# Optimization experiments

Hardware: AMD Instinct MI355X
Metric: run time of the kernel (lower is better)

The kernel has to match this reference:

```python
import jax, jax.numpy as jnp
import numpy as np

D_MODEL = 256
D_STATE = 2
BATCH = 8
SEQ = 8192


def setup_inputs() -> dict:
    key = jax.random.key(0)
    ks = jax.random.split(key, 8)
    s = 1.0 / np.sqrt(D_STATE)
    x = jax.random.normal(ks[0], (BATCH, SEQ, D_MODEL), dtype=jnp.float32)
    # stable range so exp(cumsum) stays finite at T=8192 (see notes)
    log_a_mag = -jax.random.uniform(ks[1], (D_MODEL, D_STATE), jnp.float32, 1e-5, 1e-3)
    a_phase = jax.random.uniform(ks[2], (D_MODEL, D_STATE), jnp.float32, 0.0, 2.0 * np.pi)
    B_re = jax.random.normal(ks[3], (D_MODEL, D_STATE), jnp.float32) * s
    B_im = jax.random.normal(ks[4], (D_MODEL, D_STATE), jnp.float32) * s
    C_re = jax.random.normal(ks[5], (D_MODEL, D_STATE), jnp.float32) * s
    C_im = jax.random.normal(ks[6], (D_MODEL, D_STATE), jnp.float32) * s
    D_diag = jnp.ones((D_MODEL,), jnp.float32)
    return dict(x=x, log_a_mag=log_a_mag, a_phase=a_phase, B_re=B_re, B_im=B_im,
                C_re=C_re, C_im=C_im, D_diag=D_diag)


def reference(x, log_a_mag, a_phase, B_re, B_im, C_re, C_im, D_diag):
    # x: (B, T, D); params: (D, S)
    Bsz, T, D = x.shape
    S = log_a_mag.shape[1]
    # cumulative complex log-decay along time, shape (D, S, T)
    cum_r = jnp.cumsum(jnp.broadcast_to(log_a_mag[:, :, None], (D, S, T)), axis=-1)
    cum_i = jnp.cumsum(jnp.broadcast_to(a_phase[:, :, None], (D, S, T)), axis=-1)
    x_t = jnp.swapaxes(x, 1, 2)                      # (B, D, T)
    Bu_r = B_re[None, :, :, None] * x_t[:, :, None, :]   # (B, D, S, T)
    Bu_i = B_im[None, :, :, None] * x_t[:, :, None, :]
    # exp(-cum_log_a): descale inputs
    en = jnp.exp(-cum_r)
    enr = en * jnp.cos(-cum_i)
    eni = en * jnp.sin(-cum_i)
    sr = enr * Bu_r - eni * Bu_i
    si = enr * Bu_i + eni * Bu_r
    csr = jnp.cumsum(sr, axis=-1)
    csi = jnp.cumsum(si, axis=-1)
    # exp(+cum_log_a): rescale prefix sums -> hidden states h (B, D, S, T)
    ec = jnp.exp(cum_r)
    ecr = ec * jnp.cos(cum_i)
    eci = ec * jnp.sin(cum_i)
    h_r = ecr * csr - eci * csi
    h_i = ecr * csi + eci * csr
    # output: Re(C . h) summed over state + skip D*x
    y = jnp.einsum('bdst,ds->bdt', h_r, C_re) - jnp.einsum('bdst,ds->bdt', h_i, C_im)
    y = jnp.swapaxes(y, 1, 2) + D_diag * x           # (B, T, D)
    return y
```

## Files before the change

kernel.cpp:

```cpp
#include <hip/hip_runtime.h>
#include <math.h>

#define BATCH  8
#define SEQ    8192
#define DMODEL 256
#define DSTATE 2
#define CHUNKS 256
#define CLEN   32
#define CPAD   1040
#define NSEG   16
#define SEGLEN 16


__global__ __launch_bounds__(256, 8)
void ssm_chunk_state(const float* __restrict__ x,
                     const float* __restrict__ lam,
                     const float* __restrict__ aph,
                     const float* __restrict__ Bre,
                     const float* __restrict__ Bim,
                     float* __restrict__ E) {
    const int d   = threadIdx.x;
    const int bid = blockIdx.x;
    const int b   = bid >> 8;
    const int c   = bid & (CHUNKS - 1);

    const float2 lm2 = *reinterpret_cast<const float2*>(lam + d * 2);
    const float2 ph2 = *reinterpret_cast<const float2*>(aph + d * 2);
    const float2 br2 = *reinterpret_cast<const float2*>(Bre + d * 2);
    const float2 bi2 = *reinterpret_cast<const float2*>(Bim + d * 2);
    const float m0 = expf(lm2.x), m1 = expf(lm2.y);
    const float ar0 = m0 * cosf(ph2.x), ai0 = m0 * sinf(ph2.x);
    const float ar1 = m1 * cosf(ph2.y), ai1 = m1 * sinf(ph2.y);
    const float br0 = br2.x, br1 = br2.y, bi0 = bi2.x, bi1 = bi2.y;

    float hr0 = 0.f, hi0 = 0.f, hr1 = 0.f, hi1 = 0.f;
    const float* xp = x + ((size_t)b * SEQ + (size_t)c * CLEN) * DMODEL + d;
#pragma unroll 8
    for (int t = 0; t < CLEN; ++t) {
        const float xt = xp[(size_t)t * DMODEL];
        const float bx0 = br0 * xt, by0 = bi0 * xt;
        const float bx1 = br1 * xt, by1 = bi1 * xt;
        const float n0r = fmaf(ar0, hr0, fmaf(-ai0, hi0, bx0));
        const float n0i = fmaf(ar0, hi0, fmaf( ai0, hr0, by0));
        const float n1r = fmaf(ar1, hr1, fmaf(-ai1, hi1, bx1));
        const float n1i = fmaf(ar1, hi1, fmaf( ai1, hr1, by1));
        hr0 = n0r; hi0 = n0i; hr1 = n1r; hi1 = n1i;
    }

    float4 ev;
    ev.x = hr0; ev.y = hi0; ev.z = hr1; ev.w = hi1;
    *reinterpret_cast<float4*>(E + ((size_t)b * CHUNKS + c) * CPAD + d * 4) = ev;
}

__global__ __launch_bounds__(256, 4)
void ssm_seg_aggregate(const float* __restrict__ E,
                       const float* __restrict__ lam,
                       const float* __restrict__ aph,
                       float* __restrict__ G) {
    const int bid  = blockIdx.x;
    const int b    = bid >> 5;
    const int seg  = (bid >> 1) & (NSEG - 1);
    const int r    = ((bid & 1) << 8) + threadIdx.x;
    const int d    = r >> 1;
    const int s    = r & 1;

    const double lm = (double)lam[d * 2 + s];
    const double ph = (double)aph[d * 2 + s];
    const double mL = exp(lm * (double)CLEN);
    const double pL = ph * (double)CLEN;
    const float Ar = (float)(mL * cos(pL));
    const float Ai = (float)(mL * sin(pL));

    const size_t ebase =
        ((size_t)b * CHUNKS + (size_t)seg * SEGLEN) * CPAD + (size_t)r * 2;

    float2 e[SEGLEN];
#pragma unroll
    for (int i = 0; i < SEGLEN; ++i)
        e[i] = *reinterpret_cast<const float2*>(E + ebase + (size_t)i * CPAD);

    float vr = e[0].x, vi = e[0].y;
#pragma unroll
    for (int i = 1; i < SEGLEN; ++i) {
        const float nr = fmaf(Ar, vr, fmaf(-Ai, vi, e[i].x));
        const float ni = fmaf(Ar, vi, fmaf( Ai, vr, e[i].y));
        vr = nr; vi = ni;
    }

    *reinterpret_cast<float2*>(G + (((size_t)b * NSEG + seg) * 512 + r) * 2) =
        make_float2(vr, vi);
}

__global__ __launch_bounds__(256, 4)
void ssm_seg_scan(const float* __restrict__ E,
                  const float* __restrict__ G,
                  const float* __restrict__ lam,
                  const float* __restrict__ aph,
                  float* __restrict__ Hin) {
    const int bid  = blockIdx.x;
    const int b    = bid >> 5;
    const int seg  = (bid >> 1) & (NSEG - 1);
    const int r    = ((bid & 1) << 8) + threadIdx.x;
    const int d    = r >> 1;
    const int s    = r & 1;

    const double lm = (double)lam[d * 2 + s];
    const double ph = (double)aph[d * 2 + s];
    const double mL = exp(lm * (double)CLEN);
    const double pL = ph * (double)CLEN;
    const float Ar = (float)(mL * cos(pL));
    const float Ai = (float)(mL * sin(pL));
    const double mS = exp(lm * (double)(CLEN * SEGLEN));
    const double pS = ph * (double)(CLEN * SEGLEN);
    const float Sr = (float)(mS * cos(pS));
    const float Si = (float)(mS * sin(pS));

    float2 g[NSEG];
#pragma unroll
    for (int k = 0; k < NSEG; ++k)
        g[k] = *reinterpret_cast<const float2*>(
            G + (((size_t)b * NSEG + k) * 512 + r) * 2);

    const size_t ebase =
        ((size_t)b * CHUNKS + (size_t)seg * SEGLEN) * CPAD + (size_t)r * 2;
    float2 e[SEGLEN];
#pragma unroll
    for (int i = 0; i < SEGLEN; ++i)
        e[i] = *reinterpret_cast<const float2*>(E + ebase + (size_t)i * CPAD);

    float pr = 0.f, pi = 0.f;
#pragma unroll
    for (int k = 0; k < NSEG; ++k) {
        if (k < seg) {
            const float nr = fmaf(Sr, pr, fmaf(-Si, pi, g[k].x));
            const float ni = fmaf(Sr, pi, fmaf( Si, pr, g[k].y));
            pr = nr; pi = ni;
        }
    }

#pragma unroll
    for (int i = 0; i < SEGLEN; ++i) {
        *reinterpret_cast<float2*>(Hin + ebase + (size_t)i * CPAD) =
            make_float2(pr, pi);
        const float nr = fmaf(Ar, pr, fmaf(-Ai, pi, e[i].x));
        const float ni = fmaf(Ar, pi, fmaf( Ai, pr, e[i].y));
        pr = nr; pi = ni;
    }
}

__global__ __launch_bounds__(256, 8)
void ssm_output(const float* __restrict__ x,
                const float* __restrict__ lam,
                const float* __restrict__ aph,
                const float* __restrict__ Bre,
                const float* __restrict__ Bim,
                const float* __restrict__ Cre,
                const float* __restrict__ Cim,
                const float* __restrict__ Dd,
                const float* __restrict__ Hin,
                float* __restrict__ y) {
    const int d   = threadIdx.x;
    const int bid = blockIdx.x;
    const int b   = bid >> 8;
    const int c   = bid & (CHUNKS - 1);

    const float4 hv = *reinterpret_cast<const float4*>(
        Hin + ((size_t)b * CHUNKS + c) * CPAD + d * 4);
    float hr0 = hv.x, hi0 = hv.y, hr1 = hv.z, hi1 = hv.w;

    const float2 lm2 = *reinterpret_cast<const float2*>(lam + d * 2);
    const float2 ph2 = *reinterpret_cast<const float2*>(aph + d * 2);
    const float2 br2 = *reinterpret_cast<const float2*>(Bre + d * 2);
    const float2 bi2 = *reinterpret_cast<const float2*>(Bim + d * 2);
    const float2 cr2 = *reinterpret_cast<const float2*>(Cre + d * 2);
    const float2 ci2 = *reinterpret_cast<const float2*>(Cim + d * 2);
    const float dd  = Dd[d];
    const float m0 = expf(lm2.x), m1 = expf(lm2.y);
    const float ar0 = m0 * cosf(ph2.x), ai0 = m0 * sinf(ph2.x);
    const float ar1 = m1 * cosf(ph2.y), ai1 = m1 * sinf(ph2.y);
    const float br0 = br2.x, br1 = br2.y, bi0 = bi2.x, bi1 = bi2.y;
    const float cr0 = cr2.x, cr1 = cr2.y, ci0 = ci2.x, ci1 = ci2.y;

    const size_t tbase = ((size_t)b * SEQ + (size_t)c * CLEN) * DMODEL + d;
    const float* xp = x + tbase;
    float* yp = y + tbase;
#pragma unroll 8
    for (int t = 0; t < CLEN; ++t) {
        const float xt = xp[(size_t)t * DMODEL];
        const float n0r = fmaf(ar0, hr0, fmaf(-ai0, hi0, br0 * xt));
        const float n0i = fmaf(ar0, hi0, fmaf( ai0, hr0, bi0 * xt));
        const float n1r = fmaf(ar1, hr1, fmaf(-ai1, hi1, br1 * xt));
        const float n1i = fmaf(ar1, hi1, fmaf( ai1, hr1, bi1 * xt));
        hr0 = n0r; hi0 = n0i; hr1 = n1r; hi1 = n1i;
        float acc = dd * xt;
        acc = fmaf(cr0, n0r, acc);
        acc = fmaf(-ci0, n0i, acc);
        acc = fmaf(cr1, n1r, acc);
        acc = fmaf(-ci1, n1i, acc);
        __builtin_nontemporal_store(acc, yp + (size_t)t * DMODEL);
    }
}

extern "C" void kernel_launch(void* const* d_in, const int* in_sizes, int n_in,
                              void* d_out, int out_size, void* d_ws, size_t ws_size,
                              hipStream_t stream) {
    const float* x   = (const float*)d_in[0];
    const float* lam = (const float*)d_in[1];
    const float* aph = (const float*)d_in[2];
    const float* Bre = (const float*)d_in[3];
    const float* Bim = (const float*)d_in[4];
    const float* Cre = (const float*)d_in[5];
    const float* Cim = (const float*)d_in[6];
    const float* Dd  = (const float*)d_in[7];
    float* yo = (float*)d_out;

    float* E   = (float*)d_ws;
    float* Hin = E + (size_t)BATCH * CHUNKS * CPAD;
    float* G   = Hin + (size_t)BATCH * CHUNKS * CPAD;

    ssm_chunk_state<<<BATCH * CHUNKS, 256, 0, stream>>>(x, lam, aph, Bre, Bim, E);
    ssm_seg_aggregate<<<BATCH * NSEG * 2, 256, 0, stream>>>(E, lam, aph, G);
    ssm_seg_scan<<<BATCH * NSEG * 2, 256, 0, stream>>>(E, G, lam, aph, Hin);
    ssm_output<<<BATCH * CHUNKS, 256, 0, stream>>>(x, lam, aph, Bre, Bim,
                                                   Cre, Cim, Dd, Hin, yo);
}
```

Baseline: 145.2 us.

## Fuse segment scan into output kernel, recomputing chunk prefix per block

Removes the separate seg_scan kernel and the Hin workspace. Each output block now rebuilds its own starting state by scanning the segment aggregates G and the earlier chunk states E in its segment. It derives the chunk and segment decay powers by repeated double-precision squaring of the per-step decay. This saves one launch and a full write and read of Hin, but adds up to about 30 serial dependent loads and FMAs per block before the main loop, plus some double-precision work.

```diff
diff --git a/kernel.cpp b/kernel.cpp
--- a/kernel.cpp
+++ b/kernel.cpp
@@ -10,6 +10,7 @@
 #define CPAD   1040
 #define NSEG   16
 #define SEGLEN 16
+#define GROW   1040
 
 
 __global__ __launch_bounds__(256, 8)
@@ -38,12 +39,10 @@
 #pragma unroll 8
     for (int t = 0; t < CLEN; ++t) {
         const float xt = xp[(size_t)t * DMODEL];
-        const float bx0 = br0 * xt, by0 = bi0 * xt;
-        const float bx1 = br1 * xt, by1 = bi1 * xt;
-        const float n0r = fmaf(ar0, hr0, fmaf(-ai0, hi0, bx0));
-        const float n0i = fmaf(ar0, hi0, fmaf( ai0, hr0, by0));
-        const float n1r = fmaf(ar1, hr1, fmaf(-ai1, hi1, bx1));
-        const float n1i = fmaf(ar1, hi1, fmaf( ai1, hr1, by1));
+        const float n0r = fmaf(ar0, hr0, fmaf(-ai0, hi0, br0 * xt));
+        const float n0i = fmaf(ar0, hi0, fmaf( ai0, hr0, bi0 * xt));
+        const float n1r = fmaf(ar1, hr1, fmaf(-ai1, hi1, br1 * xt));
+        const float n1i = fmaf(ar1, hi1, fmaf( ai1, hr1, bi1 * xt));
         hr0 = n0r; hi0 = n0i; hr1 = n1r; hi1 = n1i;
     }
 
@@ -87,65 +86,8 @@
         vr = nr; vi = ni;
     }
 
-    *reinterpret_cast<float2*>(G + (((size_t)b * NSEG + seg) * 512 + r) * 2) =
+    *reinterpret_cast<float2*>(G + ((size_t)b * NSEG + seg) * GROW + r * 2) =
         make_float2(vr, vi);
-}
-
-__global__ __launch_bounds__(256, 4)
-void ssm_seg_scan(const float* __restrict__ E,
-                  const float* __restrict__ G,
-                  const float* __restrict__ lam,
-                  const float* __restrict__ aph,
-                  float* __restrict__ Hin) {
-    const int bid  = blockIdx.x;
-    const int b    = bid >> 5;
-    const int seg  = (bid >> 1) & (NSEG - 1);
-    const int r    = ((bid & 1) << 8) + threadIdx.x;
-    const int d    = r >> 1;
-    const int s    = r & 1;
-
-    const double lm = (double)lam[d * 2 + s];
-    const double ph = (double)aph[d * 2 + s];
-    const double mL = exp(lm * (double)CLEN);
-    const double pL = ph * (double)CLEN;
-    const float Ar = (float)(mL * cos(pL));
-    const float Ai = (float)(mL * sin(pL));
-    const double mS = exp(lm * (double)(CLEN * SEGLEN));
-    const double pS = ph * (double)(CLEN * SEGLEN);
-    const float Sr = (float)(mS * cos(pS));
-    const float Si = (float)(mS * sin(pS));
-
-    float2 g[NSEG];
-#pragma unroll
-    for (int k = 0; k < NSEG; ++k)
-        g[k] = *reinterpret_cast<const float2*>(
-            G + (((size_t)b * NSEG + k) * 512 + r) * 2);
-
-    const size_t ebase =
-        ((size_t)b * CHUNKS + (size_t)seg * SEGLEN) * CPAD + (size_t)r * 2;
-    float2 e[SEGLEN];
-#pragma unroll
-    for (int i = 0; i < SEGLEN; ++i)
-        e[i] = *reinterpret_cast<const float2*>(E + ebase + (size_t)i * CPAD);
-
-    float pr = 0.f, pi = 0.f;
-#pragma unroll
-    for (int k = 0; k < NSEG; ++k) {
-        if (k < seg) {
-            const float nr = fmaf(Sr, pr, fmaf(-Si, pi, g[k].x));
-            const float ni = fmaf(Sr, pi, fmaf( Si, pr, g[k].y));
-            pr = nr; pi = ni;
-        }
-    }
-
-#pragma unroll
-    for (int i = 0; i < SEGLEN; ++i) {
-        *reinterpret_cast<float2*>(Hin + ebase + (size_t)i * CPAD) =
-            make_float2(pr, pi);
-        const float nr = fmaf(Ar, pr, fmaf(-Ai, pi, e[i].x));
-        const float ni = fmaf(Ar, pi, fmaf( Ai, pr, e[i].y));
-        pr = nr; pi = ni;
-    }
 }
 
 __global__ __launch_bounds__(256, 8)
@@ -157,16 +99,15 @@
                 const float* __restrict__ Cre,
                 const float* __restrict__ Cim,
                 const float* __restrict__ Dd,
-                const float* __restrict__ Hin,
+                const float* __restrict__ E,
+                const float* __restrict__ G,
                 float* __restrict__ y) {
     const int d   = threadIdx.x;
     const int bid = blockIdx.x;
     const int b   = bid >> 8;
     const int c   = bid & (CHUNKS - 1);
-
-    const float4 hv = *reinterpret_cast<const float4*>(
-        Hin + ((size_t)b * CHUNKS + c) * CPAD + d * 4);
-    float hr0 = hv.x, hi0 = hv.y, hr1 = hv.z, hi1 = hv.w;
+    const int seg = c >> 4;
+    const int i   = c & (SEGLEN - 1);
 
     const float2 lm2 = *reinterpret_cast<const float2*>(lam + d * 2);
     const float2 ph2 = *reinterpret_cast<const float2*>(aph + d * 2);
@@ -180,6 +121,45 @@
     const float ar1 = m1 * cosf(ph2.y), ai1 = m1 * sinf(ph2.y);
     const float br0 = br2.x, br1 = br2.y, bi0 = bi2.x, bi1 = bi2.y;
     const float cr0 = cr2.x, cr1 = cr2.y, ci0 = ci2.x, ci1 = ci2.y;
+
+    double w0r = (double)ar0, w0i = (double)ai0;
+    double w1r = (double)ar1, w1i = (double)ai1;
+#pragma unroll
+    for (int q = 0; q < 5; ++q) {
+        double t0 = w0r * w0r - w0i * w0i; w0i = 2.0 * w0r * w0i; w0r = t0;
+        double t1 = w1r * w1r - w1i * w1i; w1i = 2.0 * w1r * w1i; w1r = t1;
+    }
+    const float AL0r = (float)w0r, AL0i = (float)w0i;
+    const float AL1r = (float)w1r, AL1i = (float)w1i;
+#pragma unroll
+    for (int q = 0; q < 4; ++q) {
+        double t0 = w0r * w0r - w0i * w0i; w0i = 2.0 * w0r * w0i; w0r = t0;
+        double t1 = w1r * w1r - w1i * w1i; w1i = 2.0 * w1r * w1i; w1r = t1;
+    }
+    const float AS0r = (float)w0r, AS0i = (float)w0i;
+    const float AS1r = (float)w1r, AS1i = (float)w1i;
+
+    float P0r = 0.f, P0i = 0.f, P1r = 0.f, P1i = 0.f;
+    const float* gp = G + (size_t)b * NSEG * GROW + d * 4;
+    for (int k = 0; k < seg; ++k) {
+        const float4 gv = *reinterpret_cast<const float4*>(gp + (size_t)k * GROW);
+        const float n0r = fmaf(AS0r, P0r, fmaf(-AS0i, P0i, gv.x));
+        const float n0i = fmaf(AS0r, P0i, fmaf( AS0i, P0r, gv.y));
+        const float n1r = fmaf(AS1r, P1r, fmaf(-AS1i, P1i, gv.z));
+        const float n1i = fmaf(AS1r, P1i, fmaf( AS1i, P1r, gv.w));
+        P0r = n0r; P0i = n0i; P1r = n1r; P1i = n1i;
+    }
+    const float* ep = E + ((size_t)b * CHUNKS + (size_t)seg * SEGLEN) * CPAD + d * 4;
+    for (int j = 0; j < i; ++j) {
+        const float4 ev = *reinterpret_cast<const float4*>(ep + (size_t)j * CPAD);
+        const float n0r = fmaf(AL0r, P0r, fmaf(-AL0i, P0i, ev.x));
+        const float n0i = fmaf(AL0r, P0i, fmaf( AL0i, P0r, ev.y));
+        const float n1r = fmaf(AL1r, P1r, fmaf(-AL1i, P1i, ev.z));
+        const float n1i = fmaf(AL1r, P1i, fmaf( AL1i, P1r, ev.w));
+        P0r = n0r; P0i = n0i; P1r = n1r; P1i = n1i;
+    }
+
+    float hr0 = P0r, hi0 = P0i, hr1 = P1r, hi1 = P1i;
 
     const size_t tbase = ((size_t)b * SEQ + (size_t)c * CLEN) * DMODEL + d;
     const float* xp = x + tbase;
@@ -214,13 +194,11 @@
     const float* Dd  = (const float*)d_in[7];
     float* yo = (float*)d_out;
 
-    float* E   = (float*)d_ws;
-    float* Hin = E + (size_t)BATCH * CHUNKS * CPAD;
-    float* G   = Hin + (size_t)BATCH * CHUNKS * CPAD;
+    float* E = (float*)d_ws;
+    float* G = E + (size_t)BATCH * CHUNKS * CPAD;
 
     ssm_chunk_state<<<BATCH * CHUNKS, 256, 0, stream>>>(x, lam, aph, Bre, Bim, E);
     ssm_seg_aggregate<<<BATCH * NSEG * 2, 256, 0, stream>>>(E, lam, aph, G);
-    ssm_seg_scan<<<BATCH * NSEG * 2, 256, 0, stream>>>(E, G, lam, aph, Hin);
     ssm_output<<<BATCH * CHUNKS, 256, 0, stream>>>(x, lam, aph, Bre, Bim,
-                                                   Cre, Cim, Dd, Hin, yo);
-}
+                                                   Cre, Cim, Dd, E, G, yo);
+}
```

Measured after the change: 148.6 us. +2.3%, slower.
